# Performance work log

Hardware: AMD Instinct MI355X
Metric: run time of the kernel (lower is better)

The kernel has to match this reference:

```python
import jax, jax.numpy as jnp
import numpy as np

B, S, D = 8, 1024, 1024

def setup_inputs() -> dict:
    key = jax.random.key(0)
    ks = jax.random.split(key, 6)
    context = jax.random.normal(ks[0], (B, S, D), dtype=jnp.float32)
    eos_mask = jax.random.randint(ks[1], (B, S), 0, 2, dtype=jnp.int32)
    prior = jax.random.uniform(ks[2], (), dtype=jnp.float32)
    adj_mat = jax.random.randint(ks[3], (B, S, S), 0, 2, dtype=jnp.int32)
    Wk = jax.random.normal(ks[4], (D, D), dtype=jnp.float32) * 0.02
    Wq = jax.random.normal(ks[5], (D, D), dtype=jnp.float32) * 0.02
    bk = jnp.zeros((D,), jnp.float32)
    bq = jnp.zeros((D,), jnp.float32)
    ln_gamma = jnp.ones((D,), jnp.float32)
    ln_beta = jnp.zeros((D,), jnp.float32)
    return {"context": context, "eos_mask": eos_mask, "prior": prior,
            "adj_mat": adj_mat, "Wk": Wk, "bk": bk, "Wq": Wq, "bq": bq,
            "ln_gamma": ln_gamma, "ln_beta": ln_beta}

def reference(context, eos_mask, prior, adj_mat, Wk, bk, Wq, bq, ln_gamma, ln_beta):
    d_model = context.shape[-1]
    seq_len = context.shape[1]
    # LayerNorm (annotated-transformer style: unbiased std, eps added to std)
    mu = jnp.mean(context, axis=-1, keepdims=True)
    std = jnp.std(context, axis=-1, keepdims=True, ddof=1)
    x = ln_gamma * (context - mu) / (std + 1e-6) + ln_beta
    # projections (torch Linear: x @ W.T + b)
    key_p = x @ Wk.T + bk
    query = x @ Wq.T + bq
    scores = jnp.einsum('bqd,bkd->bqk', query, key_p) / (d_model / 2)
    scores = jnp.where(adj_mat == 0, -1e9, scores)
    neibor_attn = jax.nn.softmax(scores, axis=-1)
    neibor_attn = jnp.sqrt(neibor_attn * jnp.swapaxes(neibor_attn, -1, -2) + 1e-9)
    neibor_attn = prior + (1.0 - prior) * neibor_attn
    # constant structural matrices
    a = jnp.eye(seq_len, k=1, dtype=jnp.float32)          # superdiagonal
    b = jnp.eye(seq_len, dtype=jnp.float32)               # diagonal
    tri = jnp.triu(jnp.ones((seq_len, seq_len), jnp.float32))  # upper incl diag
    # t = (log(attn+eps) masked to superdiagonal) @ tri
    t = jnp.matmul(jnp.where(a == 0, 0.0, jnp.log(neibor_attn + 1e-9)), tri)
    g_attn = jnp.exp(jnp.matmul(tri, t))
    g_attn = jnp.where((tri - b) == 0, 0.0, g_attn)  # keep strict upper only
    g_attn = g_attn + jnp.swapaxes(g_attn, -1, -2) + jnp.where(b == 0, 1e-9, neibor_attn)
    return (g_attn, neibor_attn)
```

## Files before the change

### kernel.cpp

```cpp
#include <hip/hip_runtime.h>
#include <hip/hip_bf16.h>

#define S_LEN 1024
#define D_DIM 1024
#define N_BAT 8
#define BSS   (8ull*1024ull*1024ull)

using bf16x8 = __attribute__((ext_vector_type(8))) short;
using f32x4  = __attribute__((ext_vector_type(4))) float;

__device__ __forceinline__ short f2bf(float v) {
    __hip_bfloat16 h = __float2bfloat16(v);
    return *reinterpret_cast<short*>(&h);
}

__device__ __forceinline__ void gload_lds16(const void* g, void* l) {
    __builtin_amdgcn_global_load_lds(
        (const __attribute__((address_space(1))) void*)g,
        (__attribute__((address_space(3))) void*)l, 16, 0, 0);
}

#define RDFRAG(slot, AF, BF)                                                  \
    {                                                                         \
        const char* _Ac = (const char*)As + (slot) * 32768;                   \
        const char* _Bc = (const char*)Bs + (slot) * 16384;                   \
        _Pragma("unroll")                                                     \
        for (int _m = 0; _m < 4; ++_m) {                                      \
            const int _row = wr * 64 + _m * 16 + rsel;                        \
            _Pragma("unroll")                                                 \
            for (int _kk = 0; _kk < 2; ++_kk)                                 \
                AF[_m][_kk] = *(const bf16x8*)&_Ac[_row * 128 +               \
                                                  ((_kk * 64 + kb) ^ sw)];    \
        }                                                                     \
        _Pragma("unroll")                                                     \
        for (int _n = 0; _n < 4; ++_n) {                                      \
            const int _row = wc * 64 + _n * 16 + rsel;                        \
            _Pragma("unroll")                                                 \
            for (int _kk = 0; _kk < 2; ++_kk)                                 \
                BF[_n][_kk] = *(const bf16x8*)&_Bc[_row * 128 +               \
                                                  ((_kk * 64 + kb) ^ sw)];    \
        }                                                                     \
    }

#define MMA_ALL(AF, BF)                                                       \
    __builtin_amdgcn_s_setprio(1);                                            \
    _Pragma("unroll")                                                         \
    for (int _kk = 0; _kk < 2; ++_kk)                                         \
        _Pragma("unroll")                                                     \
        for (int _m = 0; _m < 4; ++_m)                                        \
            _Pragma("unroll")                                                  \
            for (int _n = 0; _n < 4; ++_n)                                    \
                acc[_m][_n] = __builtin_amdgcn_mfma_f32_16x16x32_bf16(        \
                    AF[_m][_kk], BF[_n][_kk], acc[_m][_n], 0, 0, 0);          \
    __builtin_amdgcn_s_setprio(0);

template<int KITERS>
__device__ __forceinline__ void gemm_mainloop256(
    const short* __restrict__ A, const short* __restrict__ Bt,
    int brow, int bcol, int kstart,
    short* As, short* Bs, f32x4 acc[4][4])
{
    const int tid  = threadIdx.x;
    const int lane = tid & 63;
    const int w    = tid >> 6;
    const int wr   = w >> 1;
    const int wc   = w & 1;
    const int rsel = lane & 15;
    const int kb   = (lane >> 4) * 16;
    const int sw   = (rsel & 7) << 4;

    const int srow  = tid >> 3;
    const int scolb = ((tid & 7) * 16) ^ ((srow & 7) << 4);
    const int sdst  = tid * 16;

#pragma unroll
    for (int m = 0; m < 4; ++m)
#pragma unroll
        for (int n = 0; n < 4; ++n) acc[m][n] = 0.0f;

    auto stage = [&](int slot, int k0) {
        char* Ad = (char*)As + slot * 32768;
        char* Bd = (char*)Bs + slot * 16384;
#pragma unroll
        for (int c = 0; c < 4; ++c) {
            const int row = c * 64 + srow;
            gload_lds16((const char*)(A + (size_t)(brow + row) * 1024 + k0) + scolb,
                        Ad + c * 8192 + sdst);
        }
#pragma unroll
        for (int c = 0; c < 2; ++c) {
            const int row = c * 64 + srow;
            gload_lds16((const char*)(Bt + (size_t)(bcol + row) * 1024 + k0) + scolb,
                        Bd + c * 8192 + sdst);
        }
    };

    stage(0, kstart);
    if (KITERS > 1) {
        stage(1, kstart + 64);
        asm volatile("s_waitcnt vmcnt(6)" ::: "memory");
    } else {
        asm volatile("s_waitcnt vmcnt(0)" ::: "memory");
    }
    __builtin_amdgcn_s_barrier();
    asm volatile("" ::: "memory");

    bf16x8 af0[4][2], bf0[4][2], af1[4][2], bf1[4][2];
    RDFRAG(0, af0, bf0);

#pragma unroll
    for (int t = 0; t < KITERS; ++t) {
        if (t + 2 < KITERS) stage((t + 2) % 3, kstart + (t + 2) * 64);
        if (t + 2 < KITERS)      asm volatile("s_waitcnt vmcnt(6)" ::: "memory");
        else if (t + 1 < KITERS) asm volatile("s_waitcnt vmcnt(0)" ::: "memory");
        if (t + 1 < KITERS) {
            asm volatile("s_waitcnt lgkmcnt(0)" ::: "memory");
            __builtin_amdgcn_s_barrier();
            asm volatile("" ::: "memory");
            if ((t & 1) == 0) { RDFRAG((t + 1) % 3, af1, bf1); }
            else              { RDFRAG((t + 1) % 3, af0, bf0); }
        }
        if ((t & 1) == 0) { MMA_ALL(af0, bf0); }
        else              { MMA_ALL(af1, bf1); }
    }
}

__global__ __launch_bounds__(512) void gemm_bf16(
    const short* __restrict__ A, const short* __restrict__ Bt,
    short* __restrict__ C)
{
    __shared__ short As[3 * 16384];
    __shared__ short Bs[3 * 8192];
    const int flat = blockIdx.x + 32 * blockIdx.y;
    const int nid  = (flat & 7) * 32 + (flat >> 3);
    const int mx   = nid >> 3;
    const int ny   = nid & 7;
    const int brow = mx * 256, bcol = ny * 128;

    f32x4 acc[4][4];
    gemm_mainloop256<16>(A, Bt, brow, bcol, 0, As, Bs, acc);

    const int lane = threadIdx.x & 63;
    const int w    = threadIdx.x >> 6;
    const int wr   = w >> 1, wc = w & 1;
#pragma unroll
    for (int m = 0; m < 4; ++m)
#pragma unroll
        for (int n = 0; n < 4; ++n) {
            const int colg = bcol + wc * 64 + n * 16 + (lane & 15);
#pragma unroll
            for (int r = 0; r < 4; ++r) {
                const int rowg = brow + wr * 64 + m * 16 + ((lane >> 4) * 4 + r);
                C[(size_t)rowg * 1024 + colg] = f2bf(acc[m][n][r]);
            }
        }
}

__global__ __launch_bounds__(512) void gemm_scores(
    const short* __restrict__ Tm, const short* __restrict__ Xm,
    const float* __restrict__ p, const float* __restrict__ r2,
    const float* __restrict__ c0p, const int* __restrict__ adj,
    float* __restrict__ Sc)
{
    __shared__ short As[3 * 16384];
    __shared__ short Bs[3 * 8192];
    const int flat = blockIdx.x + 4 * blockIdx.y + 32 * blockIdx.z;
    const int nid  = (flat & 7) * 32 + (flat >> 3);
    const int b    = nid >> 5;
    const int rem  = nid & 31;
    const int mx   = rem & 3;
    const int ny   = rem >> 2;
    const short* A  = Tm + (size_t)b * 1024 * 1024;
    const short* Bt = Xm + (size_t)b * 1024 * 1024;
    const float* pb = p  + (size_t)b * 1024;
    const float* rb = r2 + (size_t)b * 1024;
    const int*   ab = adj + (size_t)b * 1024 * 1024;
    float* C = Sc + (size_t)b * 1024 * 1024;
    const int brow = mx * 256, bcol = ny * 128;

    f32x4 acc[4][4];
    gemm_mainloop256<16>(A, Bt, brow, bcol, 0, As, Bs, acc);

    const int lane = threadIdx.x & 63;
    const int w    = threadIdx.x >> 6;
    const int wr   = w >> 1, wc = w & 1;
    const float c0v = c0p[0];
#pragma unroll
    for (int m = 0; m < 4; ++m)
#pragma unroll
        for (int n = 0; n < 4; ++n) {
            const int colg = bcol + wc * 64 + n * 16 + (lane & 15);
            const float radd = rb[colg] + c0v;
#pragma unroll
            for (int r = 0; r < 4; ++r) {
                const int rowg = brow + wr * 64 + m * 16 + ((lane >> 4) * 4 + r);
                const size_t idx = (size_t)rowg * 1024 + colg;
                const float val = (acc[m][n][r] + pb[rowg] + radd) * 0.001953125f;
                C[idx] = ab[idx] ? val : -1e9f;
            }
        }
}

__global__ __launch_bounds__(512) void gemm_splitk(
    const short* __restrict__ A, const short* __restrict__ Bt,
    float* __restrict__ P)
{
    __shared__ short As[3 * 16384];
    __shared__ short Bs[3 * 8192];
    const int brow = blockIdx.x * 256, bcol = blockIdx.y * 128;
    const int z = blockIdx.z;

    f32x4 acc[4][4];
    gemm_mainloop256<4>(A, Bt, brow, bcol, z * 256, As, Bs, acc);

    float* Pz = P + (size_t)z * 1024 * 1024;
    const int lane = threadIdx.x & 63;
    const int w    = threadIdx.x >> 6;
    const int wr   = w >> 1, wc = w & 1;
#pragma unroll
    for (int m = 0; m < 4; ++m)
#pragma unroll
        for (int n = 0; n < 4; ++n) {
            const int colg = bcol + wc * 64 + n * 16 + (lane & 15);
#pragma unroll
            for (int r = 0; r < 4; ++r) {
                const int rowg = brow + wr * 64 + m * 16 + ((lane >> 4) * 4 + r);
                Pz[(size_t)rowg * 1024 + colg] = acc[m][n][r];
            }
        }
}

__global__ __launch_bounds__(256) void reduce_m2t(
    const float* __restrict__ P, short* __restrict__ M)
{
    const int idx = blockIdx.x * 256 + threadIdx.x;
    const float4* P4 = (const float4*)P;
    float4 s = P4[idx];
    const float4 s1 = P4[idx + 262144];
    const float4 s2 = P4[idx + 524288];
    const float4 s3 = P4[idx + 786432];
    s.x += s1.x + s2.x + s3.x;
    s.y += s1.y + s2.y + s3.y;
    s.z += s1.z + s2.z + s3.z;
    s.w += s1.w + s2.w + s3.w;
    short4 o;
    o.x = f2bf(s.x); o.y = f2bf(s.y); o.z = f2bf(s.z); o.w = f2bf(s.w);
    ((short4*)M)[idx] = o;
}

__global__ __launch_bounds__(256) void bias_gemv1(
    const float* __restrict__ Wq, const float* __restrict__ Wk,
    const float* __restrict__ bk, const float* __restrict__ bq,
    float* __restrict__ pu, float* __restrict__ pv)
{
    __shared__ float su[8][128];
    __shared__ float sv[8][128];
    const int tx = threadIdx.x & 31;
    const int ty = threadIdx.x >> 5;
    const int colBase = blockIdx.x * 128;
    const int rowBase = blockIdx.y * 64;
    const int i = colBase + tx * 4;
    float4 au = {0,0,0,0}, av = {0,0,0,0};
#pragma unroll
    for (int jj = 0; jj < 8; ++jj) {
        const int j = rowBase + ty + jj * 8;
        const float bkv = bk[j], bqv = bq[j];
        const float4 wq = *(const float4*)&Wq[(size_t)j * 1024 + i];
        const float4 wk = *(const float4*)&Wk[(size_t)j * 1024 + i];
        au.x += wq.x * bkv; au.y += wq.y * bkv; au.z += wq.z * bkv; au.w += wq.w * bkv;
        av.x += wk.x * bqv; av.y += wk.y * bqv; av.z += wk.z * bqv; av.w += wk.w * bqv;
    }
    ((float4*)su[ty])[tx] = au;
    ((float4*)sv[ty])[tx] = av;
    __syncthreads();
    if (ty == 0) {
        float4 s1 = ((float4*)su[0])[tx];
        float4 s2 = ((float4*)sv[0])[tx];
#pragma unroll
        for (int k = 1; k < 8; ++k) {
            const float4 t1 = ((float4*)su[k])[tx];
            const float4 t2 = ((float4*)sv[k])[tx];
            s1.x += t1.x; s1.y += t1.y; s1.z += t1.z; s1.w += t1.w;
            s2.x += t2.x; s2.y += t2.y; s2.z += t2.z; s2.w += t2.w;
        }
        ((float4*)&pu[(size_t)blockIdx.y * 1024 + colBase])[tx] = s1;
        ((float4*)&pv[(size_t)blockIdx.y * 1024 + colBase])[tx] = s2;
    }
}

__global__ __launch_bounds__(256) void bias_gemv2(
    const float* __restrict__ pu, const float* __restrict__ pv,
    const float* __restrict__ bk, const float* __restrict__ bq,
    float* __restrict__ u, float* __restrict__ v, float* __restrict__ c0)
{
    __shared__ float sh[4];
    const int i = blockIdx.x * 256 + threadIdx.x;
    float su = 0.0f, sv = 0.0f;
#pragma unroll
    for (int k = 0; k < 16; ++k) {
        su += pu[k * 1024 + i];
        sv += pv[k * 1024 + i];
    }
    u[i] = su;
    v[i] = sv;
    if (blockIdx.x == 0) {
        const int t = threadIdx.x;
        const float4 a = ((const float4*)bq)[t];
        const float4 b = ((const float4*)bk)[t];
        float s = a.x*b.x + a.y*b.y + a.z*b.z + a.w*b.w;
        for (int off = 32; off > 0; off >>= 1) s += __shfl_down(s, off);
        const int lane = t & 63, w = t >> 6;
        if (lane == 0) sh[w] = s;
        __syncthreads();
        if (t == 0) c0[0] = sh[0] + sh[1] + sh[2] + sh[3];
    }
}

__global__ __launch_bounds__(256) void ln_kernel(
    const float* __restrict__ X, const float* __restrict__ gamma,
    const float* __restrict__ beta, const float* __restrict__ u,
    const float* __restrict__ v2, short* __restrict__ Y,
    float* __restrict__ p, float* __restrict__ r2)
{
    __shared__ float sh[16];
    const size_t row = blockIdx.x;
    const int t = threadIdx.x;
    float4 v = ((const float4*)(X + row * 1024))[t];
    float s  = v.x + v.y + v.z + v.w;
    float ss = v.x*v.x + v.y*v.y + v.z*v.z + v.w*v.w;
    for (int off = 32; off > 0; off >>= 1) {
        s  += __shfl_down(s, off);
        ss += __shfl_down(ss, off);
    }
    const int lane = t & 63, w = t >> 6;
    if (lane == 0) { sh[w] = s; sh[4 + w] = ss; }
    __syncthreads();
    if (t == 0) {
        float S  = sh[0] + sh[1] + sh[2] + sh[3];
        float SS = sh[4] + sh[5] + sh[6] + sh[7];
        float mu = S * (1.0f / 1024.0f);
        float var = fmaxf((SS - S * mu) * (1.0f / 1023.0f), 0.0f);
        sh[0] = mu;
        sh[1] = 1.0f / (sqrtf(var) + 1e-6f);
    }
    __syncthreads();
    const float mu = sh[0], inv = sh[1];
    float4 g  = ((const float4*)gamma)[t];
    float4 be = ((const float4*)beta)[t];
    float y0 = g.x * (v.x - mu) * inv + be.x;
    float y1 = g.y * (v.y - mu) * inv + be.y;
    float y2 = g.z * (v.z - mu) * inv + be.z;
    float y3 = g.w * (v.w - mu) * inv + be.w;
    short4 o;
    o.x = f2bf(y0); o.y = f2bf(y1); o.z = f2bf(y2); o.w = f2bf(y3);
    ((short4*)(Y + row * 1024))[t] = o;
    float4 uu = ((const float4*)u)[t];
    float4 vv = ((const float4*)v2)[t];
    float dp = y0*uu.x + y1*uu.y + y2*uu.z + y3*uu.w;
    float dr = y0*vv.x + y1*vv.y + y2*vv.z + y3*vv.w;
    for (int off = 32; off > 0; off >>= 1) {
        dp += __shfl_down(dp, off);
        dr += __shfl_down(dr, off);
    }
    if (lane == 0) { sh[8 + w] = dp; sh[12 + w] = dr; }
    __syncthreads();
    if (t == 0) {
        p[row]  = sh[8] + sh[9] + sh[10] + sh[11];
        r2[row] = sh[12] + sh[13] + sh[14] + sh[15];
    }
}

__global__ __launch_bounds__(256) void cvt_t_kernel(
    const float* __restrict__ Wq, const float* __restrict__ Wk,
    short* __restrict__ wqt, short* __restrict__ wkt)
{
    __shared__ float T[32][33];
    const float* src = blockIdx.z ? Wk : Wq;
    short* dst = blockIdx.z ? wkt : wqt;
    const int bi = blockIdx.x * 32, bj = blockIdx.y * 32;
    const int c = threadIdx.x & 31, r0 = threadIdx.x >> 5;
#pragma unroll
    for (int rr = 0; rr < 4; ++rr) {
        const int r = r0 + rr * 8;
        T[r][c] = src[(size_t)(bi + r) * 1024 + bj + c];
    }
    __syncthreads();
#pragma unroll
    for (int rr = 0; rr < 4; ++rr) {
        const int r = r0 + rr * 8;
        dst[(size_t)(bj + r) * 1024 + bi + c] = f2bf(T[c][r]);
    }
}

__global__ __launch_bounds__(256) void rowstat_kernel(
    const float* __restrict__ Sc, float2* __restrict__ stats)
{
    __shared__ float sh[4];
    const size_t row = blockIdx.x;
    const int t = threadIdx.x;
    const float4 sv = ((const float4*)(Sc + row * 1024))[t];
    float m = fmaxf(fmaxf(sv.x, sv.y), fmaxf(sv.z, sv.w));
    for (int off = 32; off > 0; off >>= 1) m = fmaxf(m, __shfl_down(m, off));
    const int lane = t & 63, w = t >> 6;
    if (lane == 0) sh[w] = m;
    __syncthreads();
    const float M = fmaxf(fmaxf(sh[0], sh[1]), fmaxf(sh[2], sh[3]));
    __syncthreads();
    float s = expf(sv.x - M) + expf(sv.y - M) + expf(sv.z - M) + expf(sv.w - M);
    for (int off = 32; off > 0; off >>= 1) s += __shfl_down(s, off);
    if (lane == 0) sh[w] = s;
    __syncthreads();
    if (t == 0) {
        const float Sm = sh[0] + sh[1] + sh[2] + sh[3];
        stats[row] = make_float2(M, 1.0f / Sm);
    }
}

__global__ __launch_bounds__(1024) void cum2_kernel(
    const float* __restrict__ Sc, const float2* __restrict__ stats,
    const float* __restrict__ prior_p, double* __restrict__ cum)
{
    __shared__ double sh[1024];
    const int b = blockIdx.x;
    const int t = threadIdx.x;
    const float prior = *prior_p;
    const float om = 1.0f - prior;
    const float* sc = Sc + (size_t)b * 1024 * 1024;
    const float2* st = stats + (size_t)b * 1024;
    double v = 0.0;
    if (t >= 1) {
        const int k = t - 1;
        const float2 s1 = st[k], s2 = st[k + 1];
        const float a1 = expf(sc[(size_t)k * 1024 + (k + 1)] - s1.x) * s1.y;
        const float a2 = expf(sc[(size_t)(k + 1) * 1024 + k] - s2.x) * s2.y;
        const float na = prior + om * sqrtf(a1 * a2 + 1e-9f);
        v = (double)logf(na + 1e-9f);
    }
    sh[t] = v;
    __syncthreads();
#pragma unroll
    for (int off = 1; off < 1024; off <<= 1) {
        const double add = (t >= off) ? sh[t - off] : 0.0;
        __syncthreads();
        sh[t] += add;
        __syncthreads();
    }
    cum[b * 1024 + t] = sh[t];
}

__global__ __launch_bounds__(256) void na_g2_kernel(
    float* __restrict__ Sc, const float2* __restrict__ stats,
    const float* __restrict__ prior_p, const double* __restrict__ cum,
    float* __restrict__ NA)
{
    const int flat = blockIdx.x + 1024 * blockIdx.y;
    const int nid  = (flat & 7) * 1024 + (flat >> 3);
    const int b    = nid >> 10;
    const int tidx = nid & 1023;
    const int ti = tidx >> 5, tj = tidx & 31;
    if (tj < ti) return;
    const float prior = *prior_p;
    const float om = 1.0f - prior;
    float* sc = Sc + (size_t)b * 1024 * 1024;
    float* na = NA + (size_t)b * 1024 * 1024;
    const float2* st = stats + (size_t)b * 1024;
    const double* cb = cum + (size_t)b * 1024;
    __shared__ float T1[32][33];
    __shared__ float T2[32][33];
    const int c = threadIdx.x & 31, r0 = threadIdx.x >> 5;
#pragma unroll
    for (int rr = 0; rr < 4; ++rr) {
        const int r = r0 + rr * 8;
        const int R1 = ti * 32 + r, R2 = tj * 32 + r;
        const float2 s1 = st[R1], s2 = st[R2];
        T1[r][c] = expf(sc[(size_t)R1 * 1024 + tj * 32 + c] - s1.x) * s1.y;
        T2[r][c] = expf(sc[(size_t)R2 * 1024 + ti * 32 + c] - s2.x) * s2.y;
    }
    __syncthreads();
#pragma unroll
    for (int rr = 0; rr < 4; ++rr) {
        const int r = r0 + rr * 8;
        const int R1 = ti * 32 + r, C1 = tj * 32 + c;
        const float na1 = prior + om * sqrtf(T1[r][c] * T2[c][r] + 1e-9f);
        na[(size_t)R1 * 1024 + C1] = na1;
        float g1;
        if (R1 == C1) g1 = na1;
        else {
            const int lo = min(R1, C1), hi = max(R1, C1);
            g1 = expf((float)(cb[hi] - cb[lo])) + 1e-9f;
        }
        sc[(size_t)R1 * 1024 + C1] = g1;
        const int R2 = tj * 32 + r, C2 = ti * 32 + c;
        const float na2 = prior + om * sqrtf(T2[r][c] * T1[c][r] + 1e-9f);
        na[(size_t)R2 * 1024 + C2] = na2;
        float g2;
        if (R2 == C2) g2 = na2;
        else {
            const int lo = min(R2, C2), hi = max(R2, C2);
            g2 = expf((float)(cb[hi] - cb[lo])) + 1e-9f;
        }
        sc[(size_t)R2 * 1024 + C2] = g2;
    }
}

extern "C" void kernel_launch(void* const* d_in, const int* in_sizes, int n_in,
                              void* d_out, int out_size, void* d_ws, size_t ws_size,
                              hipStream_t stream)
{
    const float* context = (const float*)d_in[0];
    const float* prior   = (const float*)d_in[2];
    const int*   adj     = (const int*)d_in[3];
    const float* Wk      = (const float*)d_in[4];
    const float* bk      = (const float*)d_in[5];
    const float* Wq      = (const float*)d_in[6];
    const float* bq      = (const float*)d_in[7];
    const float* gamma   = (const float*)d_in[8];
    const float* beta    = (const float*)d_in[9];

    float* out   = (float*)d_out;
    float* gout  = out;
    float* naout = out + BSS;

    char* ws = (char*)d_ws;
    short*  xb    = (short*)(ws);
    short*  wqt   = (short*)(ws + (16ull << 20));
    short*  wkt   = (short*)(ws + (18ull << 20));
    short*  m2t   = (short*)(ws + (20ull << 20));
    short*  tb    = (short*)(ws + (22ull << 20));
    float*  m2par = (float*)tb;
    double* cumd  = (double*)(ws + (38ull << 20));
    float*  uvec  = (float*)(ws + (38ull << 20) + (1ull << 16));
    float*  vvec  = uvec + 1024;
    float*  c0    = vvec + 1024;
    float*  pvec  = c0 + 64;
    float*  rvec  = pvec + 8192;
    float*  pu    = rvec + 8192;
    float*  pv    = pu + 16384;
    float2* statv = (float2*)(pv + 16384);

    bias_gemv1<<<dim3(8, 16), 256, 0, stream>>>(Wq, Wk, bk, bq, pu, pv);
    bias_gemv2<<<4, 256, 0, stream>>>(pu, pv, bk, bq, uvec, vvec, c0);
    ln_kernel<<<8192, 256, 0, stream>>>(context, gamma, beta, uvec, vvec,
                                        xb, pvec, rvec);
    cvt_t_kernel<<<dim3(32, 32, 2), 256, 0, stream>>>(Wq, Wk, wqt, wkt);
    gemm_splitk<<<dim3(4, 8, 4), 512, 0, stream>>>(wkt, wqt, m2par);
    reduce_m2t<<<1024, 256, 0, stream>>>(m2par, m2t);
    gemm_bf16<<<dim3(32, 8), 512, 0, stream>>>(xb, m2t, tb);
    gemm_scores<<<dim3(4, 8, 8), 512, 0, stream>>>(tb, xb, pvec, rvec, c0,
                                                   adj, gout);
    rowstat_kernel<<<8192, 256, 0, stream>>>(gout, statv);
    cum2_kernel<<<8, 1024, 0, stream>>>(gout, statv, prior, cumd);
    na_g2_kernel<<<dim3(1024, 8), 256, 0, stream>>>(gout, statv, prior, cumd,
                                                    naout);
}
```

Baseline: 120.8 us.

## Pack adjacency to bitmask and stage GEMM epilogues through LDS for vector stores

A new pre-pass packs the int32 adjacency matrix into a bitmask with wave ballots. The scores GEMM then reads one 32-bit word per 32 columns instead of an int per element. The scores and bf16 GEMM epilogues now write accumulators to shared memory, then emit coalesced 16-byte row stores in place of scattered scalar stores. The extra launch still reads the full adj once. The shared buffers are enlarged to hold the epilogue tile, which may reduce occupancy or add barrier cost.

New measurement: 126.2 us. +4.4%, slower.

```diff
diff --git a/kernel.cpp b/kernel.cpp
--- a/kernel.cpp
+++ b/kernel.cpp
@@ -125,12 +125,27 @@
     }
 }
 
+__global__ __launch_bounds__(256) void pack_adj(
+    const int* __restrict__ adj, unsigned* __restrict__ mb)
+{
+    const int lane = threadIdx.x & 63;
+    const size_t wid = ((size_t)blockIdx.x * 256 + threadIdx.x) >> 6;
+    const size_t nw  = ((size_t)gridDim.x * 256) >> 6;
+    for (size_t c = wid; c < (BSS >> 6); c += nw) {
+        const int a = adj[(c << 6) + lane];
+        const unsigned long long m = __ballot(a != 0);
+        if ((lane & 31) == 0)
+            mb[(c << 1) + (lane >> 5)] = (unsigned)(m >> (lane & 32));
+    }
+}
+
 __global__ __launch_bounds__(512) void gemm_bf16(
     const short* __restrict__ A, const short* __restrict__ Bt,
     short* __restrict__ C)
 {
-    __shared__ short As[3 * 16384];
-    __shared__ short Bs[3 * 8192];
+    __shared__ char smem[147456];
+    short* As = (short*)smem;
+    short* Bs = (short*)(smem + 98304);
     const int flat = blockIdx.x + 32 * blockIdx.y;
     const int nid  = (flat & 7) * 32 + (flat >> 3);
     const int mx   = nid >> 3;
@@ -140,6 +155,8 @@
     f32x4 acc[4][4];
     gemm_mainloop256<16>(A, Bt, brow, bcol, 0, As, Bs, acc);
 
+    __syncthreads();
+    short* ep = (short*)smem;
     const int lane = threadIdx.x & 63;
     const int w    = threadIdx.x >> 6;
     const int wr   = w >> 1, wc = w & 1;
@@ -147,23 +164,33 @@
     for (int m = 0; m < 4; ++m)
 #pragma unroll
         for (int n = 0; n < 4; ++n) {
-            const int colg = bcol + wc * 64 + n * 16 + (lane & 15);
+            const int Cc = wc * 64 + n * 16 + (lane & 15);
 #pragma unroll
             for (int r = 0; r < 4; ++r) {
-                const int rowg = brow + wr * 64 + m * 16 + ((lane >> 4) * 4 + r);
-                C[(size_t)rowg * 1024 + colg] = f2bf(acc[m][n][r]);
+                const int R = wr * 64 + m * 16 + (lane >> 4) * 4 + r;
+                ep[R * 136 + Cc] = f2bf(acc[m][n][r]);
             }
         }
+    __syncthreads();
+#pragma unroll
+    for (int it = 0; it < 8; ++it) {
+        const int fl  = it * 512 + threadIdx.x;
+        const int row = fl >> 4;
+        const int c8  = fl & 15;
+        const bf16x8 v = *(const bf16x8*)&ep[row * 136 + c8 * 8];
+        *(bf16x8*)&C[(size_t)(brow + row) * 1024 + bcol + c8 * 8] = v;
+    }
 }
 
 __global__ __launch_bounds__(512) void gemm_scores(
     const short* __restrict__ Tm, const short* __restrict__ Xm,
     const float* __restrict__ p, const float* __restrict__ r2,
-    const float* __restrict__ c0p, const int* __restrict__ adj,
+    const float* __restrict__ c0p, const unsigned* __restrict__ mbase,
     float* __restrict__ Sc)
 {
-    __shared__ short As[3 * 16384];
-    __shared__ short Bs[3 * 8192];
+    __shared__ char smem[147456];
+    short* As = (short*)smem;
+    short* Bs = (short*)(smem + 98304);
     const int flat = blockIdx.x + 4 * blockIdx.y + 32 * blockIdx.z;
     const int nid  = (flat & 7) * 32 + (flat >> 3);
     const int b    = nid >> 5;
@@ -174,39 +201,58 @@
     const short* Bt = Xm + (size_t)b * 1024 * 1024;
     const float* pb = p  + (size_t)b * 1024;
     const float* rb = r2 + (size_t)b * 1024;
-    const int*   ab = adj + (size_t)b * 1024 * 1024;
+    const unsigned* mbb = mbase + (size_t)b * 32768;
     float* C = Sc + (size_t)b * 1024 * 1024;
     const int brow = mx * 256, bcol = ny * 128;
 
     f32x4 acc[4][4];
     gemm_mainloop256<16>(A, Bt, brow, bcol, 0, As, Bs, acc);
 
+    __syncthreads();
+    float* ep = (float*)smem;
     const int lane = threadIdx.x & 63;
     const int w    = threadIdx.x >> 6;
     const int wr   = w >> 1, wc = w & 1;
+#pragma unroll
+    for (int m = 0; m < 4; ++m)
+#pragma unroll
+        for (int n = 0; n < 4; ++n) {
+            const int Cc = wc * 64 + n * 16 + (lane & 15);
+#pragma unroll
+            for (int r = 0; r < 4; ++r) {
+                const int R = wr * 64 + m * 16 + (lane >> 4) * 4 + r;
+                ep[R * 132 + Cc] = acc[m][n][r];
+            }
+        }
+    __syncthreads();
     const float c0v = c0p[0];
 #pragma unroll
-    for (int m = 0; m < 4; ++m)
-#pragma unroll
-        for (int n = 0; n < 4; ++n) {
-            const int colg = bcol + wc * 64 + n * 16 + (lane & 15);
-            const float radd = rb[colg] + c0v;
-#pragma unroll
-            for (int r = 0; r < 4; ++r) {
-                const int rowg = brow + wr * 64 + m * 16 + ((lane >> 4) * 4 + r);
-                const size_t idx = (size_t)rowg * 1024 + colg;
-                const float val = (acc[m][n][r] + pb[rowg] + radd) * 0.001953125f;
-                C[idx] = ab[idx] ? val : -1e9f;
-            }
-        }
+    for (int it = 0; it < 16; ++it) {
+        const int fl   = it * 512 + threadIdx.x;
+        const int row  = fl >> 5;
+        const int col4 = fl & 31;
+        const int rowg = brow + row;
+        const int colg = bcol + col4 * 4;
+        float4 v = *(const float4*)&ep[row * 132 + col4 * 4];
+        const float4 rv = *(const float4*)&rb[colg];
+        const float pa = pb[rowg] + c0v;
+        const unsigned mw = mbb[rowg * 32 + (bcol >> 5) + (col4 >> 3)];
+        const int j0 = (col4 & 7) * 4;
+        v.x = ((mw >> (j0 + 0)) & 1) ? (v.x + pa + rv.x) * 0.001953125f : -1e9f;
+        v.y = ((mw >> (j0 + 1)) & 1) ? (v.y + pa + rv.y) * 0.001953125f : -1e9f;
+        v.z = ((mw >> (j0 + 2)) & 1) ? (v.z + pa + rv.z) * 0.001953125f : -1e9f;
+        v.w = ((mw >> (j0 + 3)) & 1) ? (v.w + pa + rv.w) * 0.001953125f : -1e9f;
+        *(float4*)&C[(size_t)rowg * 1024 + colg] = v;
+    }
 }
 
 __global__ __launch_bounds__(512) void gemm_splitk(
     const short* __restrict__ A, const short* __restrict__ Bt,
     float* __restrict__ P)
 {
-    __shared__ short As[3 * 16384];
-    __shared__ short Bs[3 * 8192];
+    __shared__ char smem[147456];
+    short* As = (short*)smem;
+    short* Bs = (short*)(smem + 98304);
     const int brow = blockIdx.x * 256, bcol = blockIdx.y * 128;
     const int z = blockIdx.z;
 
@@ -537,7 +583,9 @@
     float*  pu    = rvec + 8192;
     float*  pv    = pu + 16384;
     float2* statv = (float2*)(pv + 16384);
-
+    unsigned* mb  = (unsigned*)(ws + (39ull << 20));
+
+    pack_adj<<<2048, 256, 0, stream>>>(adj, mb);
     bias_gemv1<<<dim3(8, 16), 256, 0, stream>>>(Wq, Wk, bk, bq, pu, pv);
     bias_gemv2<<<4, 256, 0, stream>>>(pu, pv, bk, bq, uvec, vvec, c0);
     ln_kernel<<<8192, 256, 0, stream>>>(context, gamma, beta, uvec, vvec,
@@ -547,7 +595,7 @@
     reduce_m2t<<<1024, 256, 0, stream>>>(m2par, m2t);
     gemm_bf16<<<dim3(32, 8), 512, 0, stream>>>(xb, m2t, tb);
     gemm_scores<<<dim3(4, 8, 8), 512, 0, stream>>>(tb, xb, pvec, rvec, c0,
-                                                   adj, gout);
+                                                   mb, gout);
     rowstat_kernel<<<8192, 256, 0, stream>>>(gout, statv);
     cum2_kernel<<<8, 1024, 0, stream>>>(gout, statv, prior, cumd);
     na_g2_kernel<<<dim3(1024, 8), 256, 0, stream>>>(gout, statv, prior, cumd,
```
